# Optimization experiments

Measured on AMD Instinct MI355X. Metric: run time of the kernel, lower is better.

The kernel has to match this reference:

```python
import math
import jax, jax.numpy as jnp
import numpy as np

HID_DIM = 1024
N_HEAD = 16
HEAD_DIM = HID_DIM // N_HEAD
NEG_FILL = -1e9


def _alibi_slopes(n_head: int) -> np.ndarray:
    """ALiBi per-head slopes (Press et al. 2021), matching get_slopes()."""
    main = 2 ** int(math.log2(n_head))
    m = (2.0 ** (-8.0 / main)) ** np.arange(1, 1 + main)
    if main < n_head:
        intra = (2.0 ** (-4.0 / main)) ** np.arange(1, 1 + 2 * (n_head - main), 2)
        m = np.concatenate([m, intra])
    return m.astype(np.float32)  # [H]


def setup_inputs() -> dict:
    key = jax.random.key(0)
    k1, k2, k3 = jax.random.split(key, 3)
    B, S = 2, 2048
    x = jax.random.normal(k1, (B, S, HID_DIM), dtype=jnp.float32)
    mask = jnp.ones((B, S), dtype=jnp.int32)
    Wqkv = jax.random.normal(k2, (HID_DIM, 3 * HID_DIM), dtype=jnp.float32) * 0.02
    Wout = jax.random.normal(k3, (HID_DIM, HID_DIM), dtype=jnp.float32) * 0.02
    return {"x": x, "mask": mask, "Wqkv": Wqkv, "Wout": Wout}


def reference(x, mask, Wqkv, Wout):
    B, S, _ = x.shape
    qkv = x @ Wqkv  # [B,S,3*hid]
    q, k, v = jnp.split(qkv, 3, axis=-1)
    k_cache, v_cache = k, v  # current_cache (pre-reshape, [B,S,hid])

    def to_heads(t):
        return t.reshape(B, S, N_HEAD, HEAD_DIM).transpose(0, 2, 1, 3)  # [B,H,S,Dh]

    q, k, v = to_heads(q), to_heads(k), to_heads(v)

    # NOTE: original code computes self.dk but never scales QK^T by it.
    scores = jnp.einsum('bhqd,bhkd->bhqk', q, k)  # [B,H,S,S]

    # ALiBi bias: tril(j - i), zero on/above diagonal elsewhere per torch.tril
    pos = jnp.arange(S)
    alibi = jnp.tril(pos[None, :] - pos[:, None]).astype(scores.dtype)  # [S,S]
    slopes = jnp.asarray(_alibi_slopes(N_HEAD))  # [H]
    scores = scores + slopes[None, :, None, None] * alibi[None, None]

    # padding mask broadcast over key dim: mask[:,None,None,:]
    scores = jnp.where(mask[:, None, None, :] == 0, NEG_FILL, scores)

    probs = jax.nn.softmax(scores, axis=-1)
    attn = jnp.einsum('bhqk,bhkd->bhqd', probs, v)  # [B,H,S,Dh]
    attn = attn.transpose(0, 2, 1, 3).reshape(B, S, HID_DIM)
    out = attn @ Wout  # dropout is identity in eval / p=0
    return out, k_cache, v_cache
```

## Files before the change

kernel.cpp:

```cpp
#include <hip/hip_runtime.h>
#include <hip/hip_bf16.h>
#include <cstdint>
#include <cstddef>

#define HID 1024
#define NH 16
#define DH 64
#define SEQ 2048
#define BATCH 2
#define BS (BATCH*SEQ)
#define LOG2E 1.4426950408889634f
#define PADK 68

typedef __attribute__((ext_vector_type(8))) short bf16x8;
typedef __attribute__((ext_vector_type(4))) float f32x4;

static __device__ __forceinline__ float fast_exp2(float x) {
    return __builtin_amdgcn_exp2f(x);
}

static __device__ __forceinline__ short f2bf(float f) {
    union { __hip_bfloat16 h; short s; } cv;
    cv.h = __float2bfloat16(f);
    return cv.s;
}
static __device__ __forceinline__ unsigned pack2(float a, float b) {
    union { __hip_bfloat162 h2; unsigned u; } cv;
    cv.h2 = __float22bfloat162_rn(make_float2(a, b));
    return cv.u;
}

typedef const __attribute__((address_space(1))) unsigned gas_u32;
typedef __attribute__((address_space(3))) unsigned las_u32;
static __device__ __forceinline__ void gload_lds16(const short* g, short* l) {
    __builtin_amdgcn_global_load_lds((gas_u32*)g, (las_u32*)l, 16, 0, 0);
}

__global__ __launch_bounds__(256)
void prep(const float* __restrict__ Wqkv, const float* __restrict__ Wout,
          const float* __restrict__ x,
          short* __restrict__ wqkvT, short* __restrict__ woutT,
          short* __restrict__ xb)
{
    __shared__ short tl[64][66];
    const int bid = blockIdx.x;
    const int t = threadIdx.x;

    if (bid >= 1024) {
        const float4* x4 = (const float4*)x;
        uint2* xo = (uint2*)xb;
        const int base = (bid - 1024) * 4096 + t;
        #pragma unroll
        for (int i = 0; i < 16; ++i) {
            float4 f = x4[base + i*256];
            xo[base + i*256] = make_uint2(pack2(f.x, f.y), pack2(f.z, f.w));
        }
        return;
    }

    const float* W; short* WT; int Nw, K, k0, n0;
    if (bid < 768) {
        W = Wqkv; WT = wqkvT; Nw = 3072; K = 1024;
        n0 = (bid % 48) * 64; k0 = (bid / 48) * 64;
    } else {
        W = Wout; WT = woutT; Nw = 1024; K = 1024;
        int b2 = bid - 768;
        n0 = (b2 & 15) * 64; k0 = (b2 >> 4) * 64;
    }
    const int r = t >> 2, c0 = (t & 3) * 16;
    const float* src = W + (size_t)(k0 + r) * Nw + n0 + c0;
    #pragma unroll
    for (int i = 0; i < 16; i += 4) {
        float4 f = *(const float4*)(src + i);
        tl[r][c0+i+0] = f2bf(f.x); tl[r][c0+i+1] = f2bf(f.y);
        tl[r][c0+i+2] = f2bf(f.z); tl[r][c0+i+3] = f2bf(f.w);
    }
    __syncthreads();
    short* dst = WT + (size_t)(n0 + r) * K + k0 + c0;
    unsigned buf[8];
    #pragma unroll
    for (int i = 0; i < 8; ++i) {
        unsigned lo = (unsigned short)tl[c0 + 2*i    ][r];
        unsigned hi = (unsigned short)tl[c0 + 2*i + 1][r];
        buf[i] = lo | (hi << 16);
    }
    *(uint4*)dst       = *(uint4*)&buf[0];
    *((uint4*)dst + 1) = *(uint4*)&buf[4];
}

__global__ __launch_bounds__(256)
void vtrans(const float* __restrict__ vc, short* __restrict__ vt)
{
    __shared__ short tl[64][66];
    const int bid = blockIdx.x;
    const int t = threadIdx.x;
    const int st = bid & 31;
    const int h  = (bid >> 5) & 15;
    const int b  = bid >> 9;
    const int s0 = st * 64;

    const int r = t >> 2, c0 = (t & 3) * 16;
    const float* src = vc + ((size_t)(b*SEQ + s0 + r)) * HID + h*DH + c0;
    #pragma unroll
    for (int i = 0; i < 16; i += 4) {
        float4 f = *(const float4*)(src + i);
        tl[r][c0+i+0] = f2bf(f.x); tl[r][c0+i+1] = f2bf(f.y);
        tl[r][c0+i+2] = f2bf(f.z); tl[r][c0+i+3] = f2bf(f.w);
    }
    __syncthreads();
    short* dst = vt + ((size_t)((b*NH + h)*DH + r)) * SEQ + s0 + c0;
    unsigned buf[8];
    #pragma unroll
    for (int i = 0; i < 8; ++i) {
        unsigned lo = (unsigned short)tl[c0 + 2*i    ][r];
        unsigned hi = (unsigned short)tl[c0 + 2*i + 1][r];
        buf[i] = lo | (hi << 16);
    }
    *(uint4*)dst       = *(uint4*)&buf[0];
    *((uint4*)dst + 1) = *(uint4*)&buf[4];
}

template<int CMODE, int BN>
__global__ __launch_bounds__(256, 3)
void gemm_lds(const short* __restrict__ A, const short* __restrict__ Bt,
              float* __restrict__ Cf,
              float* __restrict__ kc, float* __restrict__ vc,
              short* __restrict__ qb, short* __restrict__ kb,
              int M, int N, int K)
{
    constexpr int WN = BN / 2;
    constexpr int NF = WN / 16;
    __shared__ short As[128*64];
    __shared__ short Bs[BN*64];
    const int t    = threadIdx.x;
    const int wave = t >> 6, lane = t & 63;
    const int quad = lane >> 4, l16 = lane & 15;
    const int wrow = (wave & 1) * 64, wcol = (wave >> 1) * WN;
    const int n0 = blockIdx.x * BN, m0 = blockIdx.y * 128;

    f32x4 acc[4][NF];
    #pragma unroll
    for (int mi = 0; mi < 4; ++mi)
        #pragma unroll
        for (int nj = 0; nj < NF; ++nj) acc[mi][nj] = (f32x4){0.f,0.f,0.f,0.f};

    const int lr = lane >> 3;
    const int lc = (lane & 7) * 8;
    const short* Ab = A  + (size_t)(m0 + wave*32       + lr) * K + lc;
    const short* Bb = Bt + (size_t)(n0 + wave*(BN/4)   + lr) * K + lc;
    short* AsW = As + (wave*32)      * 64;
    short* BsW = Bs + (wave*(BN/4))  * 64;

    for (int kt = 0; kt < K; kt += 64) {
        #pragma unroll
        for (int i = 0; i < 4; ++i)
            gload_lds16(Ab + (size_t)(i*8)*K + kt, AsW + i*512);
        #pragma unroll
        for (int i = 0; i < BN/32; ++i)
            gload_lds16(Bb + (size_t)(i*8)*K + kt, BsW + i*512);
        __syncthreads();

        #pragma unroll
        for (int ks = 0; ks < 2; ++ks) {
            bf16x8 af[4], bfr[NF];
            #pragma unroll
            for (int mi = 0; mi < 4; ++mi)
                af[mi] = *(const bf16x8*)&As[(wrow + mi*16 + l16)*64 + ks*32 + quad*8];
            #pragma unroll
            for (int nj = 0; nj < NF; ++nj)
                bfr[nj] = *(const bf16x8*)&Bs[(wcol + nj*16 + l16)*64 + ks*32 + quad*8];
            #pragma unroll
            for (int mi = 0; mi < 4; ++mi)
                #pragma unroll
                for (int nj = 0; nj < NF; ++nj)
                    acc[mi][nj] = __builtin_amdgcn_mfma_f32_16x16x32_bf16(
                        af[mi], bfr[nj], acc[mi][nj], 0, 0, 0);
        }
        __syncthreads();
    }

    const int region = (CMODE == 0) ? (n0 >> 10) : 0;
    #pragma unroll
    for (int mi = 0; mi < 4; ++mi) {
        int rbase = m0 + wrow + mi*16 + quad*4;
        #pragma unroll
        for (int nj = 0; nj < NF; ++nj) {
            int col = n0 + wcol + nj*16 + l16;
            if (CMODE == 1) {
                #pragma unroll
                for (int reg = 0; reg < 4; ++reg)
                    Cf[(size_t)(rbase + reg) * N + col] = acc[mi][nj][reg];
            } else {
                int c = col & 1023;
                if (region == 0) {
                    #pragma unroll
                    for (int reg = 0; reg < 4; ++reg)
                        qb[(size_t)(rbase + reg) * HID + c] = f2bf(acc[mi][nj][reg] * LOG2E);
                } else if (region == 1) {
                    #pragma unroll
                    for (int reg = 0; reg < 4; ++reg) {
                        float v = acc[mi][nj][reg];
                        kc[(size_t)(rbase + reg) * HID + c] = v;
                        if (kb) kb[(size_t)(rbase + reg) * HID + c] = f2bf(v);
                    }
                } else {
                    #pragma unroll
                    for (int reg = 0; reg < 4; ++reg)
                        vc[(size_t)(rbase + reg) * HID + c] = acc[mi][nj][reg];
                }
            }
        }
    }
}

template<bool KVB>
__global__ __launch_bounds__(256, 4)
void attn_kernel(const short* qb,
                 const short* __restrict__ kb, const short* __restrict__ vtg,
                 const float* __restrict__ kc, const float* __restrict__ vc,
                 const int*   __restrict__ mask,
                 short* attn_b)
{
    __shared__ short Ks[64*PADK];
    __shared__ short Vs[64*PADK];
    __shared__ short Ps[64*PADK];
    __shared__ float Mk[64];

    const int t    = threadIdx.x;
    const int wave = t >> 6, lane = t & 63;
    const int quad = lane >> 4, l16 = lane & 15;

    const int blk  = blockIdx.x;
    const int xcd  = blk & 7;
    const int idx  = blk >> 3;
    const int pair = xcd * 4 + (idx >> 5);
    const int qt   = idx & 31;
    const int h    = pair & 15;
    const int b    = pair >> 4;
    const int q0   = qt * 64;
    const float slope2 = exp2f(-0.5f * (float)(h + 1)) * LOG2E;
    const int* mb = mask + b * SEQ;

    const int r  = t >> 2;
    const int c0 = (t & 3) * 16;

    const int qrow0 = q0 + 16*wave + quad*4;

    bf16x8 aq[2];
    #pragma unroll
    for (int ks = 0; ks < 2; ++ks)
        aq[ks] = *(const bf16x8*)(qb + ((size_t)(b*SEQ + q0 + 16*wave + l16)) * HID
                                     + h*DH + ks*32 + quad*8);

    float ls[4];
    f32x4 Oacc[4];
    #pragma unroll
    for (int i = 0; i < 4; ++i) {
        ls[i] = 0.f;
        Oacc[i] = (f32x4){0.f,0.f,0.f,0.f};
    }

    if (KVB) {
        uint4 kr0, kr1, vr0, vr1; float mval = 0.f;
        const short* kbase = kb  + ((size_t)(b*SEQ + r)) * HID + h*DH + c0;
        const short* vbase = vtg + ((size_t)((b*NH + h)*DH + r)) * SEQ + c0;

        kr0 = *(const uint4*)(kbase);
        kr1 = *(const uint4*)(kbase + 8);
        vr0 = *(const uint4*)(vbase);
        vr1 = *(const uint4*)(vbase + 8);
        if (t < 64) mval = (mb[t] == 0) ? -2.0e9f : 0.f;

        for (int kt = 0; kt < 32; ++kt) {
            const int j0 = kt * 64;
            __syncthreads();

            *(uint4*)&Ks[r*PADK + c0]     = kr0;
            *(uint4*)&Ks[r*PADK + c0 + 8] = kr1;
            *(uint4*)&Vs[r*PADK + c0]     = vr0;
            *(uint4*)&Vs[r*PADK + c0 + 8] = vr1;
            if (t < 64) Mk[t] = mval;

            if (kt < 31) {
                const short* kn = kbase + (size_t)(j0 + 64) * HID;
                const short* vn = vbase + (j0 + 64);
                kr0 = *(const uint4*)(kn);
                kr1 = *(const uint4*)(kn + 8);
                vr0 = *(const uint4*)(vn);
                vr1 = *(const uint4*)(vn + 8);
                if (t < 64) mval = (mb[j0 + 64 + t] == 0) ? -2.0e9f : 0.f;
            }
            __syncthreads();

            f32x4 S[4];
            #pragma unroll
            for (int nt = 0; nt < 4; ++nt) S[nt] = (f32x4){0.f,0.f,0.f,0.f};
            #pragma unroll
            for (int ks = 0; ks < 2; ++ks) {
                bf16x8 bk[4];
                #pragma unroll
                for (int nt = 0; nt < 4; ++nt)
                    bk[nt] = *(const bf16x8*)&Ks[(nt*16 + l16)*PADK + ks*32 + quad*8];
                __builtin_amdgcn_s_setprio(1);
                #pragma unroll
                for (int nt = 0; nt < 4; ++nt)
                    S[nt] = __builtin_amdgcn_mfma_f32_16x16x32_bf16(
                        aq[ks], bk[nt], S[nt], 0, 0, 0);
                __builtin_amdgcn_s_setprio(0);
            }

            #pragma unroll
            for (int nt = 0; nt < 4; ++nt) {
                int j = j0 + nt*16 + l16;
                float mn  = Mk[nt*16 + l16];
                float fdb = (float)(j - qrow0);
                float p[4];
                #pragma unroll
                for (int reg = 0; reg < 4; ++reg) {
                    float d = fminf(fdb - (float)reg, 0.f);
                    p[reg] = fast_exp2(fmaf(slope2, d, S[nt][reg]) + mn);
                    ls[reg] += p[reg];
                }
                #pragma unroll
                for (int reg = 0; reg < 4; ++reg)
                    Ps[(16*wave + quad*4 + reg)*PADK + nt*16 + l16] = f2bf(p[reg]);
            }

            #pragma unroll
            for (int ks = 0; ks < 2; ++ks) {
                bf16x8 ap = *(const bf16x8*)&Ps[(16*wave + l16)*PADK + ks*32 + quad*8];
                bf16x8 bv[4];
                #pragma unroll
                for (int nt = 0; nt < 4; ++nt)
                    bv[nt] = *(const bf16x8*)&Vs[(nt*16 + l16)*PADK + ks*32 + quad*8];
                __builtin_amdgcn_s_setprio(1);
                #pragma unroll
                for (int nt = 0; nt < 4; ++nt)
                    Oacc[nt] = __builtin_amdgcn_mfma_f32_16x16x32_bf16(
                        ap, bv[nt], Oacc[nt], 0, 0, 0);
                __builtin_amdgcn_s_setprio(0);
            }
        }
    } else {
        for (int kt = 0; kt < 32; ++kt) {
            const int j0 = kt * 64;
            __syncthreads();
            {
                const float* src = kc + ((size_t)(b*SEQ + j0 + r)) * HID + h*DH + c0;
                #pragma unroll
                for (int i = 0; i < 16; i += 4) {
                    float4 f = *(const float4*)(src + i);
                    *(unsigned*)&Ks[r*PADK + c0 + i]     = pack2(f.x, f.y);
                    *(unsigned*)&Ks[r*PADK + c0 + i + 2] = pack2(f.z, f.w);
                }
                int kp = t & 31, db = t >> 5;
                const float* v0 = vc + ((size_t)(b*SEQ + j0 + 2*kp)) * HID + h*DH + db*8;
                const float* v1 = v0 + HID;
                float4 a0 = *(const float4*)v0, a1 = *(const float4*)(v0 + 4);
                float4 b0 = *(const float4*)v1, b1 = *(const float4*)(v1 + 4);
                float va[8]  = {a0.x,a0.y,a0.z,a0.w,a1.x,a1.y,a1.z,a1.w};
                float vb2[8] = {b0.x,b0.y,b0.z,b0.w,b1.x,b1.y,b1.z,b1.w};
                #pragma unroll
                for (int i = 0; i < 8; ++i)
                    *(unsigned*)&Vs[(db*8 + i)*PADK + 2*kp] = pack2(va[i], vb2[i]);
                if (t < 64) Mk[t] = (mb[j0 + t] == 0) ? -2.0e9f : 0.f;
            }
            __syncthreads();

            f32x4 S[4];
            #pragma unroll
            for (int nt = 0; nt < 4; ++nt) S[nt] = (f32x4){0.f,0.f,0.f,0.f};
            #pragma unroll
            for (int ks = 0; ks < 2; ++ks) {
                bf16x8 bk[4];
                #pragma unroll
                for (int nt = 0; nt < 4; ++nt)
                    bk[nt] = *(const bf16x8*)&Ks[(nt*16 + l16)*PADK + ks*32 + quad*8];
                #pragma unroll
                for (int nt = 0; nt < 4; ++nt)
                    S[nt] = __builtin_amdgcn_mfma_f32_16x16x32_bf16(
                        aq[ks], bk[nt], S[nt], 0, 0, 0);
            }

            #pragma unroll
            for (int nt = 0; nt < 4; ++nt) {
                int j = j0 + nt*16 + l16;
                float mn  = Mk[nt*16 + l16];
                float fdb = (float)(j - qrow0);
                float p[4];
                #pragma unroll
                for (int reg = 0; reg < 4; ++reg) {
                    float d = fminf(fdb - (float)reg, 0.f);
                    p[reg] = fast_exp2(fmaf(slope2, d, S[nt][reg]) + mn);
                    ls[reg] += p[reg];
                }
                #pragma unroll
                for (int reg = 0; reg < 4; ++reg)
                    Ps[(16*wave + quad*4 + reg)*PADK + nt*16 + l16] = f2bf(p[reg]);
            }

            #pragma unroll
            for (int ks = 0; ks < 2; ++ks) {
                bf16x8 ap = *(const bf16x8*)&Ps[(16*wave + l16)*PADK + ks*32 + quad*8];
                bf16x8 bv[4];
                #pragma unroll
                for (int nt = 0; nt < 4; ++nt)
                    bv[nt] = *(const bf16x8*)&Vs[(nt*16 + l16)*PADK + ks*32 + quad*8];
                #pragma unroll
                for (int nt = 0; nt < 4; ++nt)
                    Oacc[nt] = __builtin_amdgcn_mfma_f32_16x16x32_bf16(
                        ap, bv[nt], Oacc[nt], 0, 0, 0);
            }
        }
    }

    float rinv[4];
    #pragma unroll
    for (int reg = 0; reg < 4; ++reg) {
        float s0 = ls[reg];
        #pragma unroll
        for (int off = 1; off <= 8; off <<= 1) s0 += __shfl_xor(s0, off, 64);
        rinv[reg] = 1.0f / s0;
    }

    short* ap = attn_b + (size_t)b * SEQ * HID + h * DH;
    #pragma unroll
    for (int nt = 0; nt < 4; ++nt) {
        int dcol = nt*16 + l16;
        #pragma unroll
        for (int reg = 0; reg < 4; ++reg) {
            int row = q0 + 16*wave + quad*4 + reg;
            ap[(size_t)row * HID + dcol] = f2bf(Oacc[nt][reg] * rinv[reg]);
        }
    }
}

extern "C" void kernel_launch(void* const* d_in, const int* in_sizes, int n_in,
                              void* d_out, int out_size, void* d_ws, size_t ws_size,
                              hipStream_t stream)
{
    const float* x    = (const float*)d_in[0];
    const int*   mask = (const int*)  d_in[1];
    const float* Wqkv = (const float*)d_in[2];
    const float* Wout = (const float*)d_in[3];

    float* out = (float*)d_out;
    float* kc  = out + (size_t)BS * HID;
    float* vc  = kc  + (size_t)BS * HID;

    char*  ws    = (char*)d_ws;
    short* qb    = (short*)ws;
    short* wqkvT = (short*)(ws + (8u << 20));
    short* woutT = (short*)(ws + (14u << 20));
    const bool full = ws_size >= (32u << 20);
    short* kb = full ? (short*)(ws + (16u << 20)) : nullptr;
    short* vt = full ? (short*)(ws + (24u << 20)) : nullptr;

    short* xb = (short*)out;

    prep<<<dim3(1280), dim3(256), 0, stream>>>(Wqkv, Wout, x, wqkvT, woutT, xb);

    gemm_lds<0,128><<<dim3(24, 32), dim3(256), 0, stream>>>(
        xb, wqkvT, nullptr, kc, vc, qb, kb, BS, 3*HID, HID);

    if (full) {
        vtrans<<<dim3(1024), dim3(256), 0, stream>>>(vc, vt);
        attn_kernel<true><<<dim3(1024), dim3(256), 0, stream>>>(
            qb, kb, vt, kc, vc, mask, qb);
    } else {
        attn_kernel<false><<<dim3(1024), dim3(256), 0, stream>>>(
            qb, nullptr, nullptr, kc, vc, mask, qb);
    }

    gemm_lds<1,64><<<dim3(16, 32), dim3(256), 0, stream>>>(
        qb, woutT, out, nullptr, nullptr, nullptr, nullptr, BS, HID, HID);
}
```

Measured before the change: 230.4 us.

## Fuse V transpose into QKV GEMM epilogue and remap block order for XCD locality

```diff
diff --git a/kernel.cpp b/kernel.cpp
--- a/kernel.cpp
+++ b/kernel.cpp
@@ -88,44 +88,12 @@
     *((uint4*)dst + 1) = *(uint4*)&buf[4];
 }
 
-__global__ __launch_bounds__(256)
-void vtrans(const float* __restrict__ vc, short* __restrict__ vt)
-{
-    __shared__ short tl[64][66];
-    const int bid = blockIdx.x;
-    const int t = threadIdx.x;
-    const int st = bid & 31;
-    const int h  = (bid >> 5) & 15;
-    const int b  = bid >> 9;
-    const int s0 = st * 64;
-
-    const int r = t >> 2, c0 = (t & 3) * 16;
-    const float* src = vc + ((size_t)(b*SEQ + s0 + r)) * HID + h*DH + c0;
-    #pragma unroll
-    for (int i = 0; i < 16; i += 4) {
-        float4 f = *(const float4*)(src + i);
-        tl[r][c0+i+0] = f2bf(f.x); tl[r][c0+i+1] = f2bf(f.y);
-        tl[r][c0+i+2] = f2bf(f.z); tl[r][c0+i+3] = f2bf(f.w);
-    }
-    __syncthreads();
-    short* dst = vt + ((size_t)((b*NH + h)*DH + r)) * SEQ + s0 + c0;
-    unsigned buf[8];
-    #pragma unroll
-    for (int i = 0; i < 8; ++i) {
-        unsigned lo = (unsigned short)tl[c0 + 2*i    ][r];
-        unsigned hi = (unsigned short)tl[c0 + 2*i + 1][r];
-        buf[i] = lo | (hi << 16);
-    }
-    *(uint4*)dst       = *(uint4*)&buf[0];
-    *((uint4*)dst + 1) = *(uint4*)&buf[4];
-}
-
 template<int CMODE, int BN>
 __global__ __launch_bounds__(256, 3)
 void gemm_lds(const short* __restrict__ A, const short* __restrict__ Bt,
               float* __restrict__ Cf,
               float* __restrict__ kc, float* __restrict__ vc,
-              short* __restrict__ qb, short* __restrict__ kb,
+              short* __restrict__ qb, short* __restrict__ kb, short* __restrict__ vt,
               int M, int N, int K)
 {
     constexpr int WN = BN / 2;
@@ -136,7 +104,12 @@
     const int wave = t >> 6, lane = t & 63;
     const int quad = lane >> 4, l16 = lane & 15;
     const int wrow = (wave & 1) * 64, wcol = (wave >> 1) * WN;
-    const int n0 = blockIdx.x * BN, m0 = blockIdx.y * 128;
+
+    const int nx   = gridDim.x;
+    const int lin  = blockIdx.y * nx + blockIdx.x;
+    const int chunk = (nx * gridDim.y) >> 3;
+    const int virt = (lin & 7) * chunk + (lin >> 3);
+    const int n0 = (virt % nx) * BN, m0 = (virt / nx) * 128;
 
     f32x4 acc[4][NF];
     #pragma unroll
@@ -207,6 +180,13 @@
                     #pragma unroll
                     for (int reg = 0; reg < 4; ++reg)
                         vc[(size_t)(rbase + reg) * HID + c] = acc[mi][nj][reg];
+                    if (vt) {
+                        int b = rbase >> 11, s = rbase & 2047;
+                        int h = c >> 6, d = c & 63;
+                        unsigned u[2] = {pack2(acc[mi][nj][0], acc[mi][nj][1]),
+                                         pack2(acc[mi][nj][2], acc[mi][nj][3])};
+                        *(uint2*)&vt[((size_t)((b*16 + h)*64 + d)) * SEQ + s] = *(uint2*)u;
+                    }
                 }
             }
         }
@@ -461,17 +441,15 @@
     prep<<<dim3(1280), dim3(256), 0, stream>>>(Wqkv, Wout, x, wqkvT, woutT, xb);
 
     gemm_lds<0,128><<<dim3(24, 32), dim3(256), 0, stream>>>(
-        xb, wqkvT, nullptr, kc, vc, qb, kb, BS, 3*HID, HID);
-
-    if (full) {
-        vtrans<<<dim3(1024), dim3(256), 0, stream>>>(vc, vt);
+        xb, wqkvT, nullptr, kc, vc, qb, kb, vt, BS, 3*HID, HID);
+
+    if (full)
         attn_kernel<true><<<dim3(1024), dim3(256), 0, stream>>>(
             qb, kb, vt, kc, vc, mask, qb);
-    } else {
+    else
         attn_kernel<false><<<dim3(1024), dim3(256), 0, stream>>>(
             qb, nullptr, nullptr, kc, vc, mask, qb);
-    }
 
     gemm_lds<1,64><<<dim3(16, 32), dim3(256), 0, stream>>>(
-        qb, woutT, out, nullptr, nullptr, nullptr, nullptr, BS, HID, HID);
-}
+        qb, woutT, out, nullptr, nullptr, nullptr, nullptr, nullptr, BS, HID, HID);
+}
```

Result: no change. 228.5 us (-0.9%).
